# Optimization experiments

Hardware: AMD Instinct MI355X
Metric: run time of the kernel (lower is better)

## Reference

```python
import jax, jax.numpy as jnp
import numpy as np

# dims
V, D, H = 30000, 300, 300
NS, L = 10000, 32
B, NMAX, MMAX = 256, 128, 128
EPS = 0.1          # sinkhorn entropic regularizer
ITERS = 50         # fixed sinkhorn sweeps (replaces convergence check, jit-friendly)
NEG = 1e9
PAD = 0


def setup_inputs() -> dict:
    key = jax.random.key(0)
    ks = jax.random.split(key, 12)
    data = jax.random.randint(ks[0], (NS, L), 0, V, dtype=jnp.int32)
    row_idx = jax.random.randint(ks[1], (B, NMAX), 0, NS, dtype=jnp.int32)
    col_idx = jax.random.randint(ks[2], (B, MMAX), 0, NS, dtype=jnp.int32)
    row_len = jax.random.randint(ks[3], (B,), 1, NMAX + 1, dtype=jnp.int32)
    col_len = jax.random.randint(ks[4], (B,), 1, MMAX + 1, dtype=jnp.int32)
    g = lambda k, shape, fan: (jax.random.normal(k, shape, jnp.float32) / np.sqrt(fan)).astype(jnp.float32)
    return {
        'data': data, 'row_idx': row_idx, 'col_idx': col_idx,
        'row_len': row_len, 'col_len': col_len,
        'emb': g(ks[5], (V, D), D),
        'W1': g(ks[6], (D, H), D), 'b1': jnp.zeros((H,), jnp.float32),
        'W2': g(ks[7], (H, H), H), 'b2': jnp.zeros((H,), jnp.float32),
        'Wc': g(ks[8], (2 * H, H), 2 * H), 'bc': jnp.zeros((H,), jnp.float32),
        'Wcls': g(ks[9], (2 * H, H), 2 * H), 'bcls': jnp.zeros((H,), jnp.float32),
        'Wout': g(ks[10], (H, 2), H), 'bout': jnp.zeros((2,), jnp.float32),
    }


def _forward(data, row_idx, col_idx, row_len, col_len,
             emb, W1, b1, W2, b2, Wc, bc, Wcls, bcls, Wout, bout):
    # ---- Embedder: token embedding + masked mean pool over tokens ----
    tok = emb[data]                                        # [NS, L, D]
    tmask = (data != PAD).astype(tok.dtype)[..., None]     # [NS, L, 1]
    enc = (tok * tmask).sum(1) / jnp.clip(tmask.sum(1), 1.0)   # [NS, D]
    # ---- attention_forward: 2-layer FFN ----
    henc = jax.nn.relu(jax.nn.relu(enc @ W1 + b1) @ W2 + b2)   # [NS, H]
    # ---- variable-length gather + pad (scope) ----
    rows = henc[row_idx]                                   # [B, NMAX, H]
    cols = henc[col_idx]                                   # [B, MMAX, H]
    rmask = (jnp.arange(NMAX)[None, :] < row_len[:, None]).astype(henc.dtype)
    cmask = (jnp.arange(MMAX)[None, :] < col_len[:, None]).astype(henc.dtype)
    rows = rows * rmask[..., None]
    cols = cols * cmask[..., None]
    # ---- batched pairwise cosine cost ----
    rn = rows / (jnp.linalg.norm(rows, axis=-1, keepdims=True) + 1e-8)
    cn = cols / (jnp.linalg.norm(cols, axis=-1, keepdims=True) + 1e-8)
    C = 1.0 - jnp.einsum('bnd,bmd->bnm', rn, cn)           # [B, NMAX, MMAX]
    pmask = rmask[:, :, None] * cmask[:, None, :]
    Cm = jnp.where(pmask > 0, C, 1e4)
    # uniform marginals over valid rows/cols (log-domain, -inf -> -NEG on pads)
    loga = jnp.where(rmask > 0, -jnp.log(row_len.astype(C.dtype))[:, None], -NEG)
    logb = jnp.where(cmask > 0, -jnp.log(col_len.astype(C.dtype))[:, None], -NEG)
    # ---- log-domain Sinkhorn (row/col marginal rescaling) ----
    def step(carry, _):
        f, g = carry
        f = EPS * loga - EPS * jax.nn.logsumexp((g[:, None, :] - Cm) / EPS, axis=2)
        g = EPS * logb - EPS * jax.nn.logsumexp((f[:, :, None] - Cm) / EPS, axis=1)
        return (f, g), None
    (f, g), _ = jax.lax.scan(step, (jnp.zeros_like(loga), jnp.zeros_like(logb)), None, length=ITERS)
    P = jnp.exp((f[:, :, None] + g[:, None, :] - Cm) / EPS) * pmask  # [B, NMAX, MMAX]
    # ---- attend: column_alignments @ rows, row_alignments @ columns ----
    attended_row = jnp.einsum('bnm,bnd->bmd', P, rows)     # P^T @ rows
    attended_col = jnp.einsum('bnm,bmd->bnd', P, cols)     # P @ cols
    # ---- compare_forward (1 layer) + masked sum ----
    cr = jax.nn.relu(jnp.concatenate([rows, attended_col], -1) @ Wc + bc)
    cr = (cr * rmask[..., None]).sum(1)                    # [B, H]
    cc = jax.nn.relu(jnp.concatenate([cols, attended_row], -1) @ Wc + bc)
    cc = (cc * cmask[..., None]).sum(1)                    # [B, H]
    # ---- cls_forward + out ----
    z = jax.nn.relu(jnp.concatenate([cr, cc], -1) @ Wcls + bcls)
    return z @ Wout + bout                                 # [B, 2]


def reference(data, row_idx, col_idx, row_len, col_len,
              emb, W1, b1, W2, b2, Wc, bc, Wcls, bcls, Wout, bout):
    return _forward(data, row_idx, col_idx, row_len, col_len,
                    emb, W1, b1, W2, b2, Wc, bc, Wcls, bcls, Wout, bout)
```

## Files before the change

### kernel.cpp

```cpp
#include <hip/hip_runtime.h>
#include <math.h>

#define NS 10000
#define LSEQ 32
#define DDIM 300
#define HDIM 300
#define BB 256
#define NMAX 128
#define MMAX 128
#define EPSR 0.1f
#define SITERS 50
#define KPAD 320

typedef __attribute__((ext_vector_type(8))) short bf16x8;
typedef __attribute__((ext_vector_type(4))) float f32x4;

__device__ __forceinline__ ushort f2bf(float x) {
  union { float f; unsigned u; } c; c.f = x;
  unsigned r = (c.u + 0x7fffu + ((c.u >> 16) & 1u)) >> 16;
  return (ushort)r;
}
__device__ __forceinline__ float bf2f(ushort h) {
  union { unsigned u; float f; } c; c.u = ((unsigned)h) << 16;
  return c.f;
}

__global__ __launch_bounds__(256) void k_embed(const int* __restrict__ data,
                                               const float* __restrict__ emb,
                                               ushort* __restrict__ enchi,
                                               ushort* __restrict__ enclo) {
  __shared__ int ids[LSEQ];
  __shared__ __align__(16) float4 part[3][76];
  int s = blockIdx.x;
  int tid = threadIdx.x;
  if (tid < LSEQ) ids[tid] = data[s * LSEQ + tid];
  __syncthreads();
  int cnt = 0;
#pragma unroll
  for (int t = 0; t < LSEQ; ++t) cnt += (ids[t] != 0) ? 1 : 0;
  int g = tid / 75, d = tid - g * 75;
  const float4* emb4 = (const float4*)emb;
  if (g < 3) {
    float4 acc = make_float4(0.f, 0.f, 0.f, 0.f);
    for (int t = g; t < LSEQ; t += 3) {
      int id = ids[t];
      if (id != 0) {
        float4 e = emb4[(size_t)id * 75 + d];
        acc.x += e.x; acc.y += e.y; acc.z += e.z; acc.w += e.w;
      }
    }
    part[g][d] = acc;
  }
  __syncthreads();
  if (g == 0) {
    float4 a = part[0][d], b = part[1][d], c = part[2][d];
    float inv = 1.f / (float)(cnt > 0 ? cnt : 1);
    float v[4] = {(a.x + b.x + c.x) * inv, (a.y + b.y + c.y) * inv,
                  (a.z + b.z + c.z) * inv, (a.w + b.w + c.w) * inv};
    ushort4 h, l;
    h.x = f2bf(v[0]); l.x = f2bf(v[0] - bf2f(h.x));
    h.y = f2bf(v[1]); l.y = f2bf(v[1] - bf2f(h.y));
    h.z = f2bf(v[2]); l.z = f2bf(v[2] - bf2f(h.z));
    h.w = f2bf(v[3]); l.w = f2bf(v[3] - bf2f(h.w));
    *(ushort4*)&enchi[(size_t)s * KPAD + d * 4] = h;
    *(ushort4*)&enclo[(size_t)s * KPAD + d * 4] = l;
  } else if (g == 1 && d < 5) {
    ushort4 z; z.x = z.y = z.z = z.w = 0;
    *(ushort4*)&enchi[(size_t)s * KPAD + 300 + d * 4] = z;
    *(ushort4*)&enclo[(size_t)s * KPAD + 300 + d * 4] = z;
  }
}

__global__ __launch_bounds__(256) void k_cvtw(const float* __restrict__ W,
                                              ushort* __restrict__ hiT,
                                              ushort* __restrict__ loT,
                                              int K, int N, int Npad) {
  int idx = blockIdx.x * 256 + threadIdx.x;
  if (idx >= Npad * KPAD) return;
  int n = idx / KPAD, k = idx - n * KPAD;
  float v = (n < N && k < K) ? W[(size_t)k * N + n] : 0.f;
  ushort h = f2bf(v);
  hiT[idx] = h;
  loT[idx] = f2bf(v - bf2f(h));
}

__global__ __launch_bounds__(256) void k_cvtwc(const float* __restrict__ Wc,
                                               ushort* __restrict__ hiT,
                                               ushort* __restrict__ loT) {
  int idx = blockIdx.x * 256 + threadIdx.x;
  if (idx >= 640 * KPAD) return;
  int n = idx / KPAD, k = idx - n * KPAD;
  float v = 0.f;
  if (k < 300 && n < 600)
    v = (n < 300) ? Wc[(size_t)k * 300 + n]
                  : Wc[(size_t)(300 + k) * 300 + (n - 300)];
  ushort h = f2bf(v);
  hiT[idx] = h;
  loT[idx] = f2bf(v - bf2f(h));
}

__global__ __launch_bounds__(256) void k_gemm_mfma(
    const ushort* __restrict__ Ahi, const ushort* __restrict__ Alo,
    const ushort* __restrict__ BhiT, const ushort* __restrict__ BloT,
    const float* __restrict__ bias, int M, int N, int relu,
    float* __restrict__ Cf, ushort* __restrict__ Chi,
    ushort* __restrict__ Clo) {
  __shared__ __align__(16) ushort lds[4][64][40];
  int tid = threadIdx.x;
  int m0 = blockIdx.x * 64, n0 = blockIdx.y * 64;
  int row = tid >> 2, ch = tid & 3;
  bool mok = (m0 + row) < M;
  const ushort* pAh = Ahi + (size_t)(m0 + row) * KPAD + ch * 8;
  const ushort* pAl = Alo + (size_t)(m0 + row) * KPAD + ch * 8;
  const ushort* pBh = BhiT + (size_t)(n0 + row) * KPAD + ch * 8;
  const ushort* pBl = BloT + (size_t)(n0 + row) * KPAD + ch * 8;
  uint4 rAh, rAl, rBh, rBl;
  uint4 z4; z4.x = z4.y = z4.z = z4.w = 0;
  auto ld = [&](int c) {
    int o = c * 32;
    rAh = mok ? *(const uint4*)(pAh + o) : z4;
    rAl = mok ? *(const uint4*)(pAl + o) : z4;
    rBh = *(const uint4*)(pBh + o);
    rBl = *(const uint4*)(pBl + o);
  };
  auto st = [&]() {
    *(uint4*)&lds[0][row][ch * 8] = rAh;
    *(uint4*)&lds[1][row][ch * 8] = rAl;
    *(uint4*)&lds[2][row][ch * 8] = rBh;
    *(uint4*)&lds[3][row][ch * 8] = rBl;
  };
  int w = tid >> 6, lane = tid & 63;
  int q = lane >> 4, l16 = lane & 15;
  int arow = w * 16 + l16;
  f32x4 acc[4] = {{0.f, 0.f, 0.f, 0.f}, {0.f, 0.f, 0.f, 0.f},
                  {0.f, 0.f, 0.f, 0.f}, {0.f, 0.f, 0.f, 0.f}};
  ld(0); st(); __syncthreads();
  for (int c = 0; c < 10; ++c) {
    if (c < 9) ld(c + 1);
    bf16x8 ah = *(const bf16x8*)&lds[0][arow][q * 8];
    bf16x8 al = *(const bf16x8*)&lds[1][arow][q * 8];
#pragma unroll
    for (int t = 0; t < 4; ++t) {
      int brow = t * 16 + l16;
      bf16x8 bh = *(const bf16x8*)&lds[2][brow][q * 8];
      bf16x8 bl = *(const bf16x8*)&lds[3][brow][q * 8];
      acc[t] = __builtin_amdgcn_mfma_f32_16x16x32_bf16(ah, bh, acc[t], 0, 0, 0);
      acc[t] = __builtin_amdgcn_mfma_f32_16x16x32_bf16(ah, bl, acc[t], 0, 0, 0);
      acc[t] = __builtin_amdgcn_mfma_f32_16x16x32_bf16(al, bh, acc[t], 0, 0, 0);
    }
    __syncthreads();
    if (c < 9) st();
    __syncthreads();
  }
#pragma unroll
  for (int t = 0; t < 4; ++t) {
    int n = n0 + t * 16 + l16;
    bool nin = n < N;
    float bz = (bias && nin) ? bias[n] : 0.f;
#pragma unroll
    for (int r = 0; r < 4; ++r) {
      int m = m0 + w * 16 + q * 4 + r;
      if (m >= M) continue;
      float v = acc[t][r] + bz;
      if (relu) v = v > 0.f ? v : 0.f;
      if (Cf && nin) Cf[(size_t)m * N + n] = v;
      if (Chi) {
        ushort h = 0, l = 0;
        if (nin) { h = f2bf(v); l = f2bf(v - bf2f(h)); }
        Chi[(size_t)m * KPAD + n] = h;
        Clo[(size_t)m * KPAD + n] = l;
      }
    }
  }
}

__global__ __launch_bounds__(256) void k_norm_split(
    const ushort* __restrict__ hehi, const ushort* __restrict__ helo,
    ushort* __restrict__ hnhi, ushort* __restrict__ hnlo) {
  int s = blockIdx.x * 4 + (threadIdx.x >> 6);
  int lane = threadIdx.x & 63;
  if (s >= NS) return;
  const ushort* ph = hehi + (size_t)s * KPAD;
  const ushort* pl = helo + (size_t)s * KPAD;
  float x[5];
  float ss = 0.f;
#pragma unroll
  for (int q = 0; q < 5; ++q) {
    int d = lane + q * 64;
    x[q] = bf2f(ph[d]) + bf2f(pl[d]);
    ss += x[q] * x[q];
  }
#pragma unroll
  for (int off = 32; off > 0; off >>= 1) ss += __shfl_down(ss, off, 64);
  ss = __shfl(ss, 0, 64);
  float inv = 1.f / (sqrtf(ss) + 1e-8f);
  ushort* qh = hnhi + (size_t)s * KPAD;
  ushort* ql = hnlo + (size_t)s * KPAD;
#pragma unroll
  for (int q = 0; q < 5; ++q) {
    int d = lane + q * 64;
    float v = x[q] * inv;
    ushort h = f2bf(v);
    qh[d] = h;
    ql[d] = f2bf(v - bf2f(h));
  }
}

__global__ __launch_bounds__(256) void k_cost_mfma(
    const ushort* __restrict__ hnhi, const ushort* __restrict__ hnlo,
    const int* __restrict__ ridx, const int* __restrict__ cidx,
    const int* __restrict__ rlen, const int* __restrict__ clen,
    float* __restrict__ Kmat) {
  int b = blockIdx.z;
  int r0 = blockIdx.x * 64, c0 = blockIdx.y * 64;
  int rl = rlen[b], cl = clen[b];
  float* Kg = Kmat + (size_t)b * NMAX * MMAX;
  int tid = threadIdx.x;
  if (r0 >= rl || c0 >= cl) {
    for (int l = tid; l < 64 * 16; l += 256) {
      int i = l >> 4, j = (l & 15) << 2;
      *(float4*)&Kg[(size_t)(r0 + i) * MMAX + c0 + j] =
          make_float4(0.f, 0.f, 0.f, 0.f);
    }
    return;
  }
  __shared__ int rix[64], cix[64];
  __shared__ __align__(16) ushort lds[4][64][40];
  if (tid < 64) rix[tid] = ridx[b * NMAX + r0 + tid];
  else if (tid < 128) cix[tid - 64] = cidx[b * MMAX + c0 + tid - 64];
  __syncthreads();
  int row = tid >> 2, ch = tid & 3;
  const ushort* pRh = hnhi + (size_t)rix[row] * KPAD + ch * 8;
  const ushort* pRl = hnlo + (size_t)rix[row] * KPAD + ch * 8;
  const ushort* pCh = hnhi + (size_t)cix[row] * KPAD + ch * 8;
  const ushort* pCl = hnlo + (size_t)cix[row] * KPAD + ch * 8;
  uint4 rRh, rRl, rCh, rCl;
  auto ld = [&](int c) {
    int o = c * 32;
    rRh = *(const uint4*)(pRh + o);
    rRl = *(const uint4*)(pRl + o);
    rCh = *(const uint4*)(pCh + o);
    rCl = *(const uint4*)(pCl + o);
  };
  auto st = [&]() {
    *(uint4*)&lds[0][row][ch * 8] = rRh;
    *(uint4*)&lds[1][row][ch * 8] = rRl;
    *(uint4*)&lds[2][row][ch * 8] = rCh;
    *(uint4*)&lds[3][row][ch * 8] = rCl;
  };
  int w = tid >> 6, lane = tid & 63;
  int q = lane >> 4, l16 = lane & 15;
  int arow = w * 16 + l16;
  f32x4 acc[4] = {{0.f, 0.f, 0.f, 0.f}, {0.f, 0.f, 0.f, 0.f},
                  {0.f, 0.f, 0.f, 0.f}, {0.f, 0.f, 0.f, 0.f}};
  ld(0); st(); __syncthreads();
  for (int c = 0; c < 10; ++c) {
    if (c < 9) ld(c + 1);
    bf16x8 ah = *(const bf16x8*)&lds[0][arow][q * 8];
    bf16x8 al = *(const bf16x8*)&lds[1][arow][q * 8];
#pragma unroll
    for (int t = 0; t < 4; ++t) {
      int brow = t * 16 + l16;
      bf16x8 bh = *(const bf16x8*)&lds[2][brow][q * 8];
      bf16x8 bl = *(const bf16x8*)&lds[3][brow][q * 8];
      acc[t] = __builtin_amdgcn_mfma_f32_16x16x32_bf16(ah, bh, acc[t], 0, 0, 0);
      acc[t] = __builtin_amdgcn_mfma_f32_16x16x32_bf16(ah, bl, acc[t], 0, 0, 0);
      acc[t] = __builtin_amdgcn_mfma_f32_16x16x32_bf16(al, bh, acc[t], 0, 0, 0);
    }
    __syncthreads();
    if (c < 9) st();
    __syncthreads();
  }
#pragma unroll
  for (int t = 0; t < 4; ++t) {
    int n = c0 + t * 16 + l16;
#pragma unroll
    for (int r = 0; r < 4; ++r) {
      int m = r0 + w * 16 + q * 4 + r;
      float kv = (m < rl && n < cl) ? expf((acc[t][r] - 1.f) / EPSR) : 0.f;
      Kg[(size_t)m * MMAX + n] = kv;
    }
  }
}

__global__ __launch_bounds__(512) void k_sinkhorn(
    float* __restrict__ Kmat, const int* __restrict__ rlen,
    const int* __restrict__ clen) {
  __shared__ __align__(16) float vq[4][36];
  __shared__ __align__(16) float uq[4][36];
  int b = blockIdx.x;
  int tid = threadIdx.x;
  int n = tid >> 2, q = tid & 3;
  int rl = rlen[b], cl = clen[b];
  float* Kg = Kmat + (size_t)b * NMAX * MMAX;
  float kr[32], kt[32];
  const float4* Kg4 = (const float4*)(Kg + (size_t)n * MMAX + 32 * q);
#pragma unroll
  for (int t = 0; t < 8; ++t) *(float4*)&kr[4 * t] = Kg4[t];
#pragma unroll
  for (int j = 0; j < 32; ++j) kt[j] = Kg[(size_t)(32 * q + j) * MMAX + n];
  if (tid < 128) vq[tid >> 5][tid & 31] = (tid < cl) ? 1.f : 0.f;
  float av = (n < rl) ? 1.f / (float)rl : 0.f;
  float bv = (n < cl) ? 1.f / (float)cl : 0.f;
  float un = 0.f;
  __syncthreads();
  for (int it = 0; it < SITERS; ++it) {
    float s = 0.f;
#pragma unroll
    for (int t = 0; t < 8; ++t) {
      float4 vv = *(const float4*)&vq[q][4 * t];
      s += kr[4 * t + 0] * vv.x + kr[4 * t + 1] * vv.y +
           kr[4 * t + 2] * vv.z + kr[4 * t + 3] * vv.w;
    }
    s += __shfl_xor(s, 1, 64);
    s += __shfl_xor(s, 2, 64);
    un = (n < rl) ? av / s : 0.f;
    if (q == 0) uq[n >> 5][n & 31] = un;
    __syncthreads();
    float s2 = 0.f;
#pragma unroll
    for (int t = 0; t < 8; ++t) {
      float4 uu = *(const float4*)&uq[q][4 * t];
      s2 += kt[4 * t + 0] * uu.x + kt[4 * t + 1] * uu.y +
            kt[4 * t + 2] * uu.z + kt[4 * t + 3] * uu.w;
    }
    s2 += __shfl_xor(s2, 1, 64);
    s2 += __shfl_xor(s2, 2, 64);
    float vm = (n < cl) ? bv / s2 : 0.f;
    if (q == 0) vq[n >> 5][n & 31] = vm;
    __syncthreads();
  }
  float4* Pg4 = (float4*)(Kg + (size_t)n * MMAX + 32 * q);
#pragma unroll
  for (int t = 0; t < 8; ++t) {
    float4 vv = *(const float4*)&vq[q][4 * t];
    float4 p;
    p.x = un * kr[4 * t + 0] * vv.x;
    p.y = un * kr[4 * t + 1] * vv.y;
    p.z = un * kr[4 * t + 2] * vv.z;
    p.w = un * kr[4 * t + 3] * vv.w;
    Pg4[t] = p;
  }
}

template <int SIDE>
__global__ __launch_bounds__(256) void k_att_cmp(
    const float* __restrict__ P, const float* __restrict__ HcB,
    const int* __restrict__ idx_main, const int* __restrict__ idx_other,
    const int* __restrict__ len_main, const int* __restrict__ len_other,
    const float* __restrict__ bc, float* __restrict__ outacc) {
  int b = blockIdx.y;
  int c0 = blockIdx.x * 64;
  int lm = len_main[b], lo = len_other[b];
  __shared__ __align__(16) float smem[2][2][16][68];
  __shared__ int iox[NMAX];
  __shared__ int imx[NMAX];
  int tid = threadIdx.x, tx = tid & 15, ty = tid >> 4;
  int jj = tid & 63, kq = tid >> 6;
  if (tid < 128) iox[tid] = idx_other[b * NMAX + tid];
  else imx[tid - 128] = idx_main[b * NMAX + tid - 128];
  __syncthreads();
  const float* Pb = P + (size_t)b * NMAX * MMAX;
  bool cok = (c0 + jj) < HDIM;
  int nkc = (lo + 15) >> 4;
  int nmt = (lm + 63) >> 6;
  float pR[4], gR[4];
  auto loadPG = [&](int mt, int kc) {
    int m0 = mt * 64, k0 = kc * 16;
    if (SIDE == 0) {
#pragma unroll
      for (int p = 0; p < 4; ++p)
        pR[p] = Pb[(size_t)(m0 + ty + p * 16) * MMAX + k0 + tx];
    } else {
#pragma unroll
      for (int p = 0; p < 4; ++p)
        pR[p] = Pb[(size_t)(k0 + kq + p * 4) * MMAX + m0 + jj];
    }
#pragma unroll
    for (int p = 0; p < 4; ++p) {
      int row = iox[k0 + kq + p * 4];
      gR[p] = cok ? HcB[(size_t)row * 600 + 300 + c0 + jj] : 0.f;
    }
  };
  auto storePG = [&](int buf) {
    if (SIDE == 0) {
#pragma unroll
      for (int p = 0; p < 4; ++p) smem[buf][0][tx][ty + p * 16] = pR[p];
    } else {
#pragma unroll
      for (int p = 0; p < 4; ++p) smem[buf][0][kq + p * 4][jj] = pR[p];
    }
#pragma unroll
    for (int p = 0; p < 4; ++p) smem[buf][1][kq + p * 4][jj] = gR[p];
  };
  float colsum[4] = {0.f, 0.f, 0.f, 0.f};
  loadPG(0, 0);
  storePG(0);
  __syncthreads();
  int cur = 0;
  for (int mt = 0; mt < nmt; ++mt) {
    float acc[4][4] = {};
    for (int kc = 0; kc < nkc; ++kc) {
      bool last = (mt == nmt - 1) && (kc == nkc - 1);
      if (!last) {
        int nm = (kc + 1 < nkc) ? mt : mt + 1;
        int nk = (kc + 1 < nkc) ? kc + 1 : 0;
        loadPG(nm, nk);
      }
#pragma unroll
      for (int kk = 0; kk < 16; ++kk) {
        float4 av = *(const float4*)&smem[cur][0][kk][ty * 4];
        float4 gv = *(const float4*)&smem[cur][1][kk][tx * 4];
        float a[4] = {av.x, av.y, av.z, av.w};
        float g[4] = {gv.x, gv.y, gv.z, gv.w};
#pragma unroll
        for (int i = 0; i < 4; ++i)
#pragma unroll
          for (int j = 0; j < 4; ++j) acc[i][j] += a[i] * g[j];
      }
      if (!last) storePG(cur ^ 1);
      __syncthreads();
      cur ^= 1;
    }
#pragma unroll
    for (int i = 0; i < 4; ++i) {
      int mi = mt * 64 + ty * 4 + i;
      if (mi >= lm) continue;
      int hrow = imx[mi];
#pragma unroll
      for (int j = 0; j < 4; ++j) {
        int col = c0 + tx * 4 + j;
        if (col >= HDIM) continue;
        float y = acc[i][j] + HcB[(size_t)hrow * 600 + col] + bc[col];
        colsum[j] += y > 0.f ? y : 0.f;
      }
    }
  }
  __syncthreads();
  float(*red)[68] = (float(*)[68]) & smem[0][0][0][0];
#pragma unroll
  for (int j = 0; j < 4; ++j) red[ty][tx * 4 + j] = colsum[j];
  __syncthreads();
  if (tid < 64) {
    float s = 0.f;
#pragma unroll
    for (int r = 0; r < 16; ++r) s += red[r][tid];
    int col = c0 + tid;
    if (col < HDIM) outacc[(size_t)b * HDIM + col] = s;
  }
}

__global__ __launch_bounds__(320) void k_cls(
    const float* __restrict__ cr, const float* __restrict__ cc,
    const float* __restrict__ Wcls, const float* __restrict__ bcls,
    const float* __restrict__ Wout, const float* __restrict__ bout,
    float* __restrict__ out) {
  __shared__ __align__(16) float cz[2 * HDIM];
  __shared__ float zz[HDIM];
  int b = blockIdx.x, tid = threadIdx.x;
  if (tid < HDIM) {
    cz[tid] = cr[(size_t)b * HDIM + tid];
    cz[HDIM + tid] = cc[(size_t)b * HDIM + tid];
  }
  __syncthreads();
  if (tid < HDIM) {
    float acc = bcls[tid];
    for (int k4 = 0; k4 < 2 * HDIM; k4 += 4) {
      float4 c = *(const float4*)&cz[k4];
      acc += c.x * Wcls[(size_t)(k4 + 0) * HDIM + tid] +
             c.y * Wcls[(size_t)(k4 + 1) * HDIM + tid] +
             c.z * Wcls[(size_t)(k4 + 2) * HDIM + tid] +
             c.w * Wcls[(size_t)(k4 + 3) * HDIM + tid];
    }
    zz[tid] = acc > 0.f ? acc : 0.f;
  }
  __syncthreads();
  int o = tid >> 6, lane = tid & 63;
  if (o < 2) {
    float p = 0.f;
    for (int j = lane; j < HDIM; j += 64) p += zz[j] * Wout[(size_t)j * 2 + o];
#pragma unroll
    for (int off = 32; off > 0; off >>= 1) p += __shfl_down(p, off, 64);
    if (lane == 0) out[b * 2 + o] = p + bout[o];
  }
}

extern "C" void kernel_launch(void* const* d_in, const int* in_sizes, int n_in,
                              void* d_out, int out_size, void* d_ws, size_t ws_size,
                              hipStream_t stream) {
  (void)in_sizes; (void)n_in; (void)out_size; (void)ws_size;
  const int* data = (const int*)d_in[0];
  const int* row_idx = (const int*)d_in[1];
  const int* col_idx = (const int*)d_in[2];
  const int* row_len = (const int*)d_in[3];
  const int* col_len = (const int*)d_in[4];
  const float* emb = (const float*)d_in[5];
  const float* W1 = (const float*)d_in[6];
  const float* b1 = (const float*)d_in[7];
  const float* W2 = (const float*)d_in[8];
  const float* b2 = (const float*)d_in[9];
  const float* Wc = (const float*)d_in[10];
  const float* bc = (const float*)d_in[11];
  const float* Wcls = (const float*)d_in[12];
  const float* bcls = (const float*)d_in[13];
  const float* Wout = (const float*)d_in[14];
  const float* bout = (const float*)d_in[15];
  float* out = (float*)d_out;

  char* wp = (char*)d_ws;
  auto carve = [&](size_t bytes) {
    char* p = wp; wp += (bytes + 255) & ~(size_t)255; return p;
  };
  ushort* enchi = (ushort*)carve((size_t)NS * KPAD * 2);
  ushort* enclo = (ushort*)carve((size_t)NS * KPAD * 2);
  ushort* h1hi = (ushort*)carve((size_t)NS * KPAD * 2);
  ushort* h1lo = (ushort*)carve((size_t)NS * KPAD * 2);
  ushort* hehi = (ushort*)carve((size_t)NS * KPAD * 2);
  ushort* helo = (ushort*)carve((size_t)NS * KPAD * 2);
  ushort* hnhi = (ushort*)carve((size_t)NS * KPAD * 2);
  ushort* hnlo = (ushort*)carve((size_t)NS * KPAD * 2);
  ushort* W1hi = (ushort*)carve((size_t)KPAD * KPAD * 2);
  ushort* W1lo = (ushort*)carve((size_t)KPAD * KPAD * 2);
  ushort* W2hi = (ushort*)carve((size_t)KPAD * KPAD * 2);
  ushort* W2lo = (ushort*)carve((size_t)KPAD * KPAD * 2);
  ushort* Wchi = (ushort*)carve((size_t)640 * KPAD * 2);
  ushort* Wclo = (ushort*)carve((size_t)640 * KPAD * 2);
  float* HcB = (float*)carve((size_t)NS * 600 * 4);
  float* Km = (float*)carve((size_t)BB * NMAX * MMAX * 4);
  float* cr = (float*)carve((size_t)BB * HDIM * 4);
  float* cc = (float*)carve((size_t)BB * HDIM * 4);

  int gM = (NS + 63) / 64;

  k_embed<<<NS, 256, 0, stream>>>(data, emb, enchi, enclo);
  k_cvtw<<<(KPAD * KPAD + 255) / 256, 256, 0, stream>>>(W1, W1hi, W1lo, DDIM,
                                                        HDIM, KPAD);
  k_cvtw<<<(KPAD * KPAD + 255) / 256, 256, 0, stream>>>(W2, W2hi, W2lo, HDIM,
                                                        HDIM, KPAD);
  k_cvtwc<<<(640 * KPAD + 255) / 256, 256, 0, stream>>>(Wc, Wchi, Wclo);
  k_gemm_mfma<<<dim3(gM, 5), 256, 0, stream>>>(
      enchi, enclo, W1hi, W1lo, b1, NS, HDIM, 1, nullptr, h1hi, h1lo);
  k_gemm_mfma<<<dim3(gM, 5), 256, 0, stream>>>(
      h1hi, h1lo, W2hi, W2lo, b2, NS, HDIM, 1, nullptr, hehi, helo);
  k_norm_split<<<(NS + 3) / 4, 256, 0, stream>>>(hehi, helo, hnhi, hnlo);
  k_gemm_mfma<<<dim3(gM, 10), 256, 0, stream>>>(
      hehi, helo, Wchi, Wclo, nullptr, NS, 2 * HDIM, 0, HcB, nullptr, nullptr);
  k_cost_mfma<<<dim3(2, 2, BB), 256, 0, stream>>>(hnhi, hnlo, row_idx, col_idx,
                                                  row_len, col_len, Km);
  k_sinkhorn<<<BB, 512, 0, stream>>>(Km, row_len, col_len);
  k_att_cmp<0><<<dim3(5, BB), 256, 0, stream>>>(
      Km, HcB, row_idx, col_idx, row_len, col_len, bc, cr);
  k_att_cmp<1><<<dim3(5, BB), 256, 0, stream>>>(
      Km, HcB, col_idx, row_idx, col_len, row_len, bc, cc);
  k_cls<<<BB, 320, 0, stream>>>(cr, cc, Wcls, bcls, Wout, bout, out);
}
```

Measured before the change: 428.3 us.

## Enlarge GEMM and attention tiles, merge weight conversion kernels

The dense MFMA GEMM now uses 64x128 output tiles, with each wave computing a 32x64 sub-tile. The cost kernel uses 2x2 wave sub-tiles, and the attend/compare kernel handles 128 columns per block instead of 64. The three weight-conversion launches are merged into one kernel, and W1/W2 are padded to 384 rows to fit the wider N tile. The goal is more operand reuse per LDS load and fewer blocks and launches, at the cost of more registers per thread and some wasted work on padded columns.

```diff
diff --git a/kernel.cpp b/kernel.cpp
--- a/kernel.cpp
+++ b/kernel.cpp
@@ -11,6 +11,7 @@
 #define EPSR 0.1f
 #define SITERS 50
 #define KPAD 320
+#define NPADW 384
 
 typedef __attribute__((ext_vector_type(8))) short bf16x8;
 typedef __attribute__((ext_vector_type(4))) float f32x4;
@@ -71,32 +72,41 @@
   }
 }
 
-__global__ __launch_bounds__(256) void k_cvtw(const float* __restrict__ W,
-                                              ushort* __restrict__ hiT,
-                                              ushort* __restrict__ loT,
-                                              int K, int N, int Npad) {
-  int idx = blockIdx.x * 256 + threadIdx.x;
-  if (idx >= Npad * KPAD) return;
-  int n = idx / KPAD, k = idx - n * KPAD;
-  float v = (n < N && k < K) ? W[(size_t)k * N + n] : 0.f;
+__global__ __launch_bounds__(256) void k_cvt_all(
+    const float* __restrict__ W1, const float* __restrict__ W2,
+    const float* __restrict__ Wc, ushort* __restrict__ W1hi,
+    ushort* __restrict__ W1lo, ushort* __restrict__ W2hi,
+    ushort* __restrict__ W2lo, ushort* __restrict__ Wchi,
+    ushort* __restrict__ Wclo) {
+  int i = blockIdx.x * 256 + threadIdx.x;
+  const int SA = NPADW * KPAD;
+  const int SC = 640 * KPAD;
+  float v = 0.f;
+  ushort *ph, *pl;
+  int idx;
+  if (i < SA) {
+    idx = i;
+    int n = idx / KPAD, k = idx - n * KPAD;
+    if (n < HDIM && k < DDIM) v = W1[(size_t)k * HDIM + n];
+    ph = W1hi; pl = W1lo;
+  } else if (i < 2 * SA) {
+    idx = i - SA;
+    int n = idx / KPAD, k = idx - n * KPAD;
+    if (n < HDIM && k < HDIM) v = W2[(size_t)k * HDIM + n];
+    ph = W2hi; pl = W2lo;
+  } else if (i < 2 * SA + SC) {
+    idx = i - 2 * SA;
+    int n = idx / KPAD, k = idx - n * KPAD;
+    if (k < HDIM && n < 2 * HDIM)
+      v = (n < HDIM) ? Wc[(size_t)k * HDIM + n]
+                     : Wc[(size_t)(HDIM + k) * HDIM + (n - HDIM)];
+    ph = Wchi; pl = Wclo;
+  } else {
+    return;
+  }
   ushort h = f2bf(v);
-  hiT[idx] = h;
-  loT[idx] = f2bf(v - bf2f(h));
-}
-
-__global__ __launch_bounds__(256) void k_cvtwc(const float* __restrict__ Wc,
-                                               ushort* __restrict__ hiT,
-                                               ushort* __restrict__ loT) {
-  int idx = blockIdx.x * 256 + threadIdx.x;
-  if (idx >= 640 * KPAD) return;
-  int n = idx / KPAD, k = idx - n * KPAD;
-  float v = 0.f;
-  if (k < 300 && n < 600)
-    v = (n < 300) ? Wc[(size_t)k * 300 + n]
-                  : Wc[(size_t)(300 + k) * 300 + (n - 300)];
-  ushort h = f2bf(v);
-  hiT[idx] = h;
-  loT[idx] = f2bf(v - bf2f(h));
+  ph[idx] = h;
+  pl[idx] = f2bf(v - bf2f(h));
 }
 
 __global__ __launch_bounds__(256) void k_gemm_mfma(
@@ -105,48 +115,63 @@
     const float* __restrict__ bias, int M, int N, int relu,
     float* __restrict__ Cf, ushort* __restrict__ Chi,
     ushort* __restrict__ Clo) {
-  __shared__ __align__(16) ushort lds[4][64][40];
+  __shared__ __align__(16) ushort ldsA[2][64][40];
+  __shared__ __align__(16) ushort ldsB[2][128][40];
   int tid = threadIdx.x;
-  int m0 = blockIdx.x * 64, n0 = blockIdx.y * 64;
-  int row = tid >> 2, ch = tid & 3;
-  bool mok = (m0 + row) < M;
-  const ushort* pAh = Ahi + (size_t)(m0 + row) * KPAD + ch * 8;
-  const ushort* pAl = Alo + (size_t)(m0 + row) * KPAD + ch * 8;
-  const ushort* pBh = BhiT + (size_t)(n0 + row) * KPAD + ch * 8;
-  const ushort* pBl = BloT + (size_t)(n0 + row) * KPAD + ch * 8;
-  uint4 rAh, rAl, rBh, rBl;
+  int m0 = blockIdx.x * 64, n0 = blockIdx.y * 128;
+  int rowA = tid >> 2, chA = (tid & 3) * 8;
+  int rowB = tid >> 1, chB = (tid & 1) * 16;
+  bool mok = (m0 + rowA) < M;
+  const ushort* pAh = Ahi + (size_t)(m0 + rowA) * KPAD + chA;
+  const ushort* pAl = Alo + (size_t)(m0 + rowA) * KPAD + chA;
+  const ushort* pBh = BhiT + (size_t)(n0 + rowB) * KPAD + chB;
+  const ushort* pBl = BloT + (size_t)(n0 + rowB) * KPAD + chB;
+  uint4 rAh, rAl, rBh0, rBh1, rBl0, rBl1;
   uint4 z4; z4.x = z4.y = z4.z = z4.w = 0;
   auto ld = [&](int c) {
     int o = c * 32;
     rAh = mok ? *(const uint4*)(pAh + o) : z4;
     rAl = mok ? *(const uint4*)(pAl + o) : z4;
-    rBh = *(const uint4*)(pBh + o);
-    rBl = *(const uint4*)(pBl + o);
+    rBh0 = *(const uint4*)(pBh + o);
+    rBh1 = *(const uint4*)(pBh + o + 8);
+    rBl0 = *(const uint4*)(pBl + o);
+    rBl1 = *(const uint4*)(pBl + o + 8);
   };
   auto st = [&]() {
-    *(uint4*)&lds[0][row][ch * 8] = rAh;
-    *(uint4*)&lds[1][row][ch * 8] = rAl;
-    *(uint4*)&lds[2][row][ch * 8] = rBh;
-    *(uint4*)&lds[3][row][ch * 8] = rBl;
+    *(uint4*)&ldsA[0][rowA][chA] = rAh;
+    *(uint4*)&ldsA[1][rowA][chA] = rAl;
+    *(uint4*)&ldsB[0][rowB][chB] = rBh0;
+    *(uint4*)&ldsB[0][rowB][chB + 8] = rBh1;
+    *(uint4*)&ldsB[1][rowB][chB] = rBl0;
+    *(uint4*)&ldsB[1][rowB][chB + 8] = rBl1;
   };
   int w = tid >> 6, lane = tid & 63;
   int q = lane >> 4, l16 = lane & 15;
-  int arow = w * 16 + l16;
-  f32x4 acc[4] = {{0.f, 0.f, 0.f, 0.f}, {0.f, 0.f, 0.f, 0.f},
-                  {0.f, 0.f, 0.f, 0.f}, {0.f, 0.f, 0.f, 0.f}};
+  int mh = w >> 1, nh = w & 1;
+  f32x4 zf = {0.f, 0.f, 0.f, 0.f};
+  f32x4 acc[2][4];
+#pragma unroll
+  for (int s = 0; s < 2; ++s)
+#pragma unroll
+    for (int t = 0; t < 4; ++t) acc[s][t] = zf;
   ld(0); st(); __syncthreads();
   for (int c = 0; c < 10; ++c) {
     if (c < 9) ld(c + 1);
-    bf16x8 ah = *(const bf16x8*)&lds[0][arow][q * 8];
-    bf16x8 al = *(const bf16x8*)&lds[1][arow][q * 8];
+    bf16x8 ah0 = *(const bf16x8*)&ldsA[0][mh * 32 + l16][q * 8];
+    bf16x8 ah1 = *(const bf16x8*)&ldsA[0][mh * 32 + 16 + l16][q * 8];
+    bf16x8 al0 = *(const bf16x8*)&ldsA[1][mh * 32 + l16][q * 8];
+    bf16x8 al1 = *(const bf16x8*)&ldsA[1][mh * 32 + 16 + l16][q * 8];
 #pragma unroll
     for (int t = 0; t < 4; ++t) {
-      int brow = t * 16 + l16;
-      bf16x8 bh = *(const bf16x8*)&lds[2][brow][q * 8];
-      bf16x8 bl = *(const bf16x8*)&lds[3][brow][q * 8];
-      acc[t] = __builtin_amdgcn_mfma_f32_16x16x32_bf16(ah, bh, acc[t], 0, 0, 0);
-      acc[t] = __builtin_amdgcn_mfma_f32_16x16x32_bf16(ah, bl, acc[t], 0, 0, 0);
-      acc[t] = __builtin_amdgcn_mfma_f32_16x16x32_bf16(al, bh, acc[t], 0, 0, 0);
+      int brow = nh * 64 + t * 16 + l16;
+      bf16x8 bh = *(const bf16x8*)&ldsB[0][brow][q * 8];
+      bf16x8 bl = *(const bf16x8*)&ldsB[1][brow][q * 8];
+      acc[0][t] = __builtin_amdgcn_mfma_f32_16x16x32_bf16(ah0, bh, acc[0][t], 0, 0, 0);
+      acc[0][t] = __builtin_amdgcn_mfma_f32_16x16x32_bf16(ah0, bl, acc[0][t], 0, 0, 0);
+      acc[0][t] = __builtin_amdgcn_mfma_f32_16x16x32_bf16(al0, bh, acc[0][t], 0, 0, 0);
+      acc[1][t] = __builtin_amdgcn_mfma_f32_16x16x32_bf16(ah1, bh, acc[1][t], 0, 0, 0);
+      acc[1][t] = __builtin_amdgcn_mfma_f32_16x16x32_bf16(ah1, bl, acc[1][t], 0, 0, 0);
+      acc[1][t] = __builtin_amdgcn_mfma_f32_16x16x32_bf16(al1, bh, acc[1][t], 0, 0, 0);
     }
     __syncthreads();
     if (c < 9) st();
@@ -154,21 +179,24 @@
   }
 #pragma unroll
   for (int t = 0; t < 4; ++t) {
-    int n = n0 + t * 16 + l16;
+    int n = n0 + nh * 64 + t * 16 + l16;
     bool nin = n < N;
     float bz = (bias && nin) ? bias[n] : 0.f;
 #pragma unroll
-    for (int r = 0; r < 4; ++r) {
-      int m = m0 + w * 16 + q * 4 + r;
-      if (m >= M) continue;
-      float v = acc[t][r] + bz;
-      if (relu) v = v > 0.f ? v : 0.f;
-      if (Cf && nin) Cf[(size_t)m * N + n] = v;
-      if (Chi) {
-        ushort h = 0, l = 0;
-        if (nin) { h = f2bf(v); l = f2bf(v - bf2f(h)); }
-        Chi[(size_t)m * KPAD + n] = h;
-        Clo[(size_t)m * KPAD + n] = l;
+    for (int s = 0; s < 2; ++s) {
+#pragma unroll
+      for (int r = 0; r < 4; ++r) {
+        int m = m0 + mh * 32 + s * 16 + q * 4 + r;
+        if (m >= M) continue;
+        float v = acc[s][t][r] + bz;
+        if (relu) v = v > 0.f ? v : 0.f;
+        if (Cf && nin) Cf[(size_t)m * N + n] = v;
+        if (Chi && n < KPAD) {
+          ushort h = 0, l = 0;
+          if (nin) { h = f2bf(v); l = f2bf(v - bf2f(h)); }
+          Chi[(size_t)m * KPAD + n] = h;
+          Clo[(size_t)m * KPAD + n] = l;
+        }
       }
     }
   }
@@ -250,35 +278,47 @@
   };
   int w = tid >> 6, lane = tid & 63;
   int q = lane >> 4, l16 = lane & 15;
-  int arow = w * 16 + l16;
-  f32x4 acc[4] = {{0.f, 0.f, 0.f, 0.f}, {0.f, 0.f, 0.f, 0.f},
-                  {0.f, 0.f, 0.f, 0.f}, {0.f, 0.f, 0.f, 0.f}};
+  int mh = w >> 1, nh = w & 1;
+  f32x4 zf = {0.f, 0.f, 0.f, 0.f};
+  f32x4 acc[2][2];
+#pragma unroll
+  for (int s = 0; s < 2; ++s)
+#pragma unroll
+    for (int t = 0; t < 2; ++t) acc[s][t] = zf;
   ld(0); st(); __syncthreads();
   for (int c = 0; c < 10; ++c) {
     if (c < 9) ld(c + 1);
-    bf16x8 ah = *(const bf16x8*)&lds[0][arow][q * 8];
-    bf16x8 al = *(const bf16x8*)&lds[1][arow][q * 8];
-#pragma unroll
-    for (int t = 0; t < 4; ++t) {
-      int brow = t * 16 + l16;
+    bf16x8 ah0 = *(const bf16x8*)&lds[0][mh * 32 + l16][q * 8];
+    bf16x8 ah1 = *(const bf16x8*)&lds[0][mh * 32 + 16 + l16][q * 8];
+    bf16x8 al0 = *(const bf16x8*)&lds[1][mh * 32 + l16][q * 8];
+    bf16x8 al1 = *(const bf16x8*)&lds[1][mh * 32 + 16 + l16][q * 8];
+#pragma unroll
+    for (int t = 0; t < 2; ++t) {
+      int brow = nh * 32 + t * 16 + l16;
       bf16x8 bh = *(const bf16x8*)&lds[2][brow][q * 8];
       bf16x8 bl = *(const bf16x8*)&lds[3][brow][q * 8];
-      acc[t] = __builtin_amdgcn_mfma_f32_16x16x32_bf16(ah, bh, acc[t], 0, 0, 0);
-      acc[t] = __builtin_amdgcn_mfma_f32_16x16x32_bf16(ah, bl, acc[t], 0, 0, 0);
-      acc[t] = __builtin_amdgcn_mfma_f32_16x16x32_bf16(al, bh, acc[t], 0, 0, 0);
+      acc[0][t] = __builtin_amdgcn_mfma_f32_16x16x32_bf16(ah0, bh, acc[0][t], 0, 0, 0);
+      acc[0][t] = __builtin_amdgcn_mfma_f32_16x16x32_bf16(ah0, bl, acc[0][t], 0, 0, 0);
+      acc[0][t] = __builtin_amdgcn_mfma_f32_16x16x32_bf16(al0, bh, acc[0][t], 0, 0, 0);
+      acc[1][t] = __builtin_amdgcn_mfma_f32_16x16x32_bf16(ah1, bh, acc[1][t], 0, 0, 0);
+      acc[1][t] = __builtin_amdgcn_mfma_f32_16x16x32_bf16(ah1, bl, acc[1][t], 0, 0, 0);
+      acc[1][t] = __builtin_amdgcn_mfma_f32_16x16x32_bf16(al1, bh, acc[1][t], 0, 0, 0);
     }
     __syncthreads();
     if (c < 9) st();
     __syncthreads();
   }
 #pragma unroll
-  for (int t = 0; t < 4; ++t) {
-    int n = c0 + t * 16 + l16;
-#pragma unroll
-    for (int r = 0; r < 4; ++r) {
-      int m = r0 + w * 16 + q * 4 + r;
-      float kv = (m < rl && n < cl) ? expf((acc[t][r] - 1.f) / EPSR) : 0.f;
-      Kg[(size_t)m * MMAX + n] = kv;
+  for (int t = 0; t < 2; ++t) {
+    int n = c0 + nh * 32 + t * 16 + l16;
+#pragma unroll
+    for (int s = 0; s < 2; ++s) {
+#pragma unroll
+      for (int r = 0; r < 4; ++r) {
+        int m = r0 + mh * 32 + s * 16 + q * 4 + r;
+        float kv = (m < rl && n < cl) ? expf((acc[s][t][r] - 1.f) / EPSR) : 0.f;
+        Kg[(size_t)m * MMAX + n] = kv;
+      }
     }
   }
 }
@@ -350,9 +390,9 @@
     const int* __restrict__ len_main, const int* __restrict__ len_other,
     const float* __restrict__ bc, float* __restrict__ outacc) {
   int b = blockIdx.y;
-  int c0 = blockIdx.x * 64;
+  int c0 = blockIdx.x * 128;
   int lm = len_main[b], lo = len_other[b];
-  __shared__ __align__(16) float smem[2][2][16][68];
+  __shared__ __align__(16) float smem[2][3][16][68];
   __shared__ int iox[NMAX];
   __shared__ int imx[NMAX];
   int tid = threadIdx.x, tx = tid & 15, ty = tid >> 4;
@@ -361,10 +401,11 @@
   else imx[tid - 128] = idx_main[b * NMAX + tid - 128];
   __syncthreads();
   const float* Pb = P + (size_t)b * NMAX * MMAX;
-  bool cok = (c0 + jj) < HDIM;
+  bool cok0 = (c0 + jj) < HDIM;
+  bool cok1 = (c0 + 64 + jj) < HDIM;
   int nkc = (lo + 15) >> 4;
   int nmt = (lm + 63) >> 6;
-  float pR[4], gR[4];
+  float pR[4], gR[2][4];
   auto loadPG = [&](int mt, int kc) {
     int m0 = mt * 64, k0 = kc * 16;
     if (SIDE == 0) {
@@ -379,7 +420,9 @@
 #pragma unroll
     for (int p = 0; p < 4; ++p) {
       int row = iox[k0 + kq + p * 4];
-      gR[p] = cok ? HcB[(size_t)row * 600 + 300 + c0 + jj] : 0.f;
+      const float* base = HcB + (size_t)row * 600 + 300 + c0 + jj;
+      gR[0][p] = cok0 ? base[0] : 0.f;
+      gR[1][p] = cok1 ? base[64] : 0.f;
     }
   };
   auto storePG = [&](int buf) {
@@ -391,15 +434,18 @@
       for (int p = 0; p < 4; ++p) smem[buf][0][kq + p * 4][jj] = pR[p];
     }
 #pragma unroll
-    for (int p = 0; p < 4; ++p) smem[buf][1][kq + p * 4][jj] = gR[p];
+    for (int p = 0; p < 4; ++p) {
+      smem[buf][1][kq + p * 4][jj] = gR[0][p];
+      smem[buf][2][kq + p * 4][jj] = gR[1][p];
+    }
   };
-  float colsum[4] = {0.f, 0.f, 0.f, 0.f};
+  float colsum[8] = {0.f, 0.f, 0.f, 0.f, 0.f, 0.f, 0.f, 0.f};
   loadPG(0, 0);
   storePG(0);
   __syncthreads();
   int cur = 0;
   for (int mt = 0; mt < nmt; ++mt) {
-    float acc[4][4] = {};
+    float acc[4][8] = {};
     for (int kc = 0; kc < nkc; ++kc) {
       bool last = (mt == nmt - 1) && (kc == nkc - 1);
       if (!last) {
@@ -410,13 +456,14 @@
 #pragma unroll
       for (int kk = 0; kk < 16; ++kk) {
         float4 av = *(const float4*)&smem[cur][0][kk][ty * 4];
-        float4 gv = *(const float4*)&smem[cur][1][kk][tx * 4];
+        float4 g0 = *(const float4*)&smem[cur][1][kk][tx * 4];
+        float4 g1 = *(const float4*)&smem[cur][2][kk][tx * 4];
         float a[4] = {av.x, av.y, av.z, av.w};
-        float g[4] = {gv.x, gv.y, gv.z, gv.w};
+        float gg[8] = {g0.x, g0.y, g0.z, g0.w, g1.x, g1.y, g1.z, g1.w};
 #pragma unroll
         for (int i = 0; i < 4; ++i)
 #pragma unroll
-          for (int j = 0; j < 4; ++j) acc[i][j] += a[i] * g[j];
+          for (int j = 0; j < 8; ++j) acc[i][j] += a[i] * gg[j];
       }
       if (!last) storePG(cur ^ 1);
       __syncthreads();
@@ -428,25 +475,32 @@
       if (mi >= lm) continue;
       int hrow = imx[mi];
 #pragma unroll
-      for (int j = 0; j < 4; ++j) {
-        int col = c0 + tx * 4 + j;
-        if (col >= HDIM) continue;
-        float y = acc[i][j] + HcB[(size_t)hrow * 600 + col] + bc[col];
-        colsum[j] += y > 0.f ? y : 0.f;
+      for (int g = 0; g < 2; ++g) {
+#pragma unroll
+        for (int j = 0; j < 4; ++j) {
+          int col = c0 + g * 64 + tx * 4 + j;
+          if (col >= HDIM) continue;
+          float y = acc[i][g * 4 + j] + HcB[(size_t)hrow * 600 + col] + bc[col];
+          colsum[g * 4 + j] += y > 0.f ? y : 0.f;
+        }
       }
     }
   }
   __syncthreads();
   float(*red)[68] = (float(*)[68]) & smem[0][0][0][0];
 #pragma unroll
-  for (int j = 0; j < 4; ++j) red[ty][tx * 4 + j] = colsum[j];
-  __syncthreads();
-  if (tid < 64) {
-    float s = 0.f;
-#pragma unroll
-    for (int r = 0; r < 16; ++r) s += red[r][tid];
-    int col = c0 + tid;
-    if (col < HDIM) outacc[(size_t)b * HDIM + col] = s;
+  for (int g = 0; g < 2; ++g) {
+#pragma unroll
+    for (int j = 0; j < 4; ++j) red[ty][tx * 4 + j] = colsum[g * 4 + j];
+    __syncthreads();
+    if (tid < 64) {
+      float s = 0.f;
+#pragma unroll
+      for (int r = 0; r < 16; ++r) s += red[r][tid];
+      int col = c0 + g * 64 + tid;
+      if (col < HDIM) outacc[(size_t)b * HDIM + col] = s;
+    }
+    __syncthreads();
   }
 }
 
@@ -519,10 +573,10 @@
   ushort* helo = (ushort*)carve((size_t)NS * KPAD * 2);
   ushort* hnhi = (ushort*)carve((size_t)NS * KPAD * 2);
   ushort* hnlo = (ushort*)carve((size_t)NS * KPAD * 2);
-  ushort* W1hi = (ushort*)carve((size_t)KPAD * KPAD * 2);
-  ushort* W1lo = (ushort*)carve((size_t)KPAD * KPAD * 2);
-  ushort* W2hi = (ushort*)carve((size_t)KPAD * KPAD * 2);
-  ushort* W2lo = (ushort*)carve((size_t)KPAD * KPAD * 2);
+  ushort* W1hi = (ushort*)carve((size_t)NPADW * KPAD * 2);
+  ushort* W1lo = (ushort*)carve((size_t)NPADW * KPAD * 2);
+  ushort* W2hi = (ushort*)carve((size_t)NPADW * KPAD * 2);
+  ushort* W2lo = (ushort*)carve((size_t)NPADW * KPAD * 2);
   ushort* Wchi = (ushort*)carve((size_t)640 * KPAD * 2);
   ushort* Wclo = (ushort*)carve((size_t)640 * KPAD * 2);
   float* HcB = (float*)carve((size_t)NS * 600 * 4);
@@ -531,26 +585,24 @@
   float* cc = (float*)carve((size_t)BB * HDIM * 4);
 
   int gM = (NS + 63) / 64;
+  int cvtTotal = 2 * NPADW * KPAD + 640 * KPAD;
 
   k_embed<<<NS, 256, 0, stream>>>(data, emb, enchi, enclo);
-  k_cvtw<<<(KPAD * KPAD + 255) / 256, 256, 0, stream>>>(W1, W1hi, W1lo, DDIM,
-                                                        HDIM, KPAD);
-  k_cvtw<<<(KPAD * KPAD + 255) / 256, 256, 0, stream>>>(W2, W2hi, W2lo, HDIM,
-                                                        HDIM, KPAD);
-  k_cvtwc<<<(640 * KPAD + 255) / 256, 256, 0, stream>>>(Wc, Wchi, Wclo);
-  k_gemm_mfma<<<dim3(gM, 5), 256, 0, stream>>>(
+  k_cvt_all<<<(cvtTotal + 255) / 256, 256, 0, stream>>>(
+      W1, W2, Wc, W1hi, W1lo, W2hi, W2lo, Wchi, Wclo);
+  k_gemm_mfma<<<dim3(gM, 3), 256, 0, stream>>>(
       enchi, enclo, W1hi, W1lo, b1, NS, HDIM, 1, nullptr, h1hi, h1lo);
-  k_gemm_mfma<<<dim3(gM, 5), 256, 0, stream>>>(
+  k_gemm_mfma<<<dim3(gM, 3), 256, 0, stream>>>(
       h1hi, h1lo, W2hi, W2lo, b2, NS, HDIM, 1, nullptr, hehi, helo);
   k_norm_split<<<(NS + 3) / 4, 256, 0, stream>>>(hehi, helo, hnhi, hnlo);
-  k_gemm_mfma<<<dim3(gM, 10), 256, 0, stream>>>(
+  k_gemm_mfma<<<dim3(gM, 5), 256, 0, stream>>>(
       hehi, helo, Wchi, Wclo, nullptr, NS, 2 * HDIM, 0, HcB, nullptr, nullptr);
   k_cost_mfma<<<dim3(2, 2, BB), 256, 0, stream>>>(hnhi, hnlo, row_idx, col_idx,
                                                   row_len, col_len, Km);
   k_sinkhorn<<<BB, 512, 0, stream>>>(Km, row_len, col_len);
-  k_att_cmp<0><<<dim3(5, BB), 256, 0, stream>>>(
+  k_att_cmp<0><<<dim3(3, BB), 256, 0, stream>>>(
       Km, HcB, row_idx, col_idx, row_len, col_len, bc, cr);
-  k_att_cmp<1><<<dim3(5, BB), 256, 0, stream>>>(
+  k_att_cmp<1><<<dim3(3, BB), 256, 0, stream>>>(
       Km, HcB, col_idx, row_idx, col_len, row_len, bc, cc);
   k_cls<<<BB, 320, 0, stream>>>(cr, cc, Wcls, bcls, Wout, bout, out);
 }
```

Result: slower. 480.7 us (+12.2%).
